# Kernel optimization log

Measured on AMD Instinct MI355X. Metric: run time of the kernel, lower is better.

Reference implementation:

```python
import jax, jax.numpy as jnp
import numpy as np


def _binop(ei, ej):
    # diagonal linear recurrence combine: (a_i, b_i) * (a_j, b_j) -> (a_j*a_i, a_j*b_i + b_j)
    ai, bi = ei
    aj, bj = ej
    return aj * ai, aj * bi + bj


def setup_inputs() -> dict:
    key = jax.random.key(0)
    ks = jax.random.split(key, 9)
    B_, T, D_in, D_out, N = 16, 2048, 512, 512, 512
    inp = {
        "input": jax.random.normal(ks[0], (B_, T, D_in), dtype=jnp.float32),
        "D": jax.random.normal(ks[1], (D_out, D_in), dtype=jnp.float32) / np.sqrt(D_in),
        "nu_log": jax.random.normal(ks[2], (N,), dtype=jnp.float32),
        "theta_log": jax.random.normal(ks[3], (N,), dtype=jnp.float32),
        "gamma_log": jax.random.normal(ks[4], (N,), dtype=jnp.float32),
        "B_re": jax.random.normal(ks[5], (N, D_in), dtype=jnp.float32) / np.sqrt(2 * D_in),
        "B_im": jax.random.normal(ks[6], (N, D_in), dtype=jnp.float32) / np.sqrt(2 * D_in),
        "C_re": jax.random.normal(ks[7], (D_out, N), dtype=jnp.float32) / np.sqrt(N),
        "C_im": jax.random.normal(ks[8], (D_out, N), dtype=jnp.float32) / np.sqrt(N),
    }
    return inp


def reference(input, D, nu_log, theta_log, gamma_log, B_re, B_im, C_re, C_im):
    # ss_params
    lam_abs = jnp.exp(-jnp.exp(nu_log))                      # [N]
    lam_phase = jnp.exp(theta_log)                           # [N]
    lam = lam_abs * (jnp.cos(lam_phase) + 1j * jnp.sin(lam_phase))  # complex [N]
    gamma = jnp.exp(gamma_log)                               # [N]
    Bc = (B_re + 1j * B_im) * gamma[:, None]                 # [N, D_in]
    Cc = C_re + 1j * C_im                                    # [D_out, N]

    # input projection: Bu_elements [batch, T, N] (complex)
    Bu = input.astype(Bc.dtype) @ Bc.T
    lam_el = jnp.broadcast_to(lam, Bu.shape)

    # parallel associative scan over time axis (initial state is zero)
    _, states = jax.lax.associative_scan(_binop, (lam_el, Bu), axis=1)

    # readout
    y = jnp.real(states @ Cc.T) + input @ D.T                # [batch, T, D_out]
    return y
```

## Files before the change

kernel.cpp:

```cpp
#include <hip/hip_runtime.h>
#include <hip/hip_fp16.h>

typedef _Float16 f16;
typedef __attribute__((ext_vector_type(8))) _Float16 f16x8;
typedef __attribute__((ext_vector_type(2))) _Float16 f16x2;
typedef __attribute__((ext_vector_type(16))) float f32x16;

#define B_SZ 16
#define T_SZ 2048
#define DIN 512
#define DOUT 512
#define N_SZ 512
#define M_SZ (B_SZ * T_SZ)
#define NCHUNK 16
#define LCHUNK 128

__device__ __forceinline__ void gload_lds16(const void* g, void* l) {
  __builtin_amdgcn_global_load_lds(
      (const __attribute__((address_space(1))) void*)g,
      (__attribute__((address_space(3))) void*)l, 16, 0, 0);
}


__global__ void prep_all(const float* __restrict__ nu_log,
                         const float* __restrict__ theta_log,
                         const float* __restrict__ gamma_log,
                         const float* __restrict__ B_re, const float* __restrict__ B_im,
                         const float* __restrict__ C_re, const float* __restrict__ C_im,
                         const float* __restrict__ Dm, const float* __restrict__ input,
                         float2* __restrict__ lam2, float2* __restrict__ lamL2,
                         f16* __restrict__ W1, f16* __restrict__ W2,
                         f16* __restrict__ A2) {
  int b = blockIdx.x;
  if (b < 2) {
    int n = b * 256 + threadIdx.x;
    float nu = expf(nu_log[n]);
    float ph = expf(theta_log[n]);
    float la = expf(-nu);
    lam2[n] = make_float2(la * cosf(ph), la * sinf(ph));
    float laL = expf(-nu * (float)LCHUNK);
    float phL = ph * (float)LCHUNK;
    lamL2[n] = make_float2(laL * cosf(phL), laL * sinf(phL));
  } else if (b < 2 + 2048) {
    int tid = (b - 2) * 256 + threadIdx.x;
    int np = tid >> 9;
    int d = tid & 511;
    int n = np >> 1;
    float g = expf(gamma_log[n]);
    const float* src = (np & 1) ? B_im : B_re;
    W1[(size_t)np * 512 + d] = (f16)(src[(size_t)n * 512 + d] * g);
  } else if (b < 2 + 2048 + 3072) {
    int tid = (b - 2050) * 256 + threadIdx.x;
    int j = tid / 1536;
    int k = tid - j * 1536;
    float v;
    if (k < 512)       v =  C_re[(size_t)j * 512 + k];
    else if (k < 1024) v = -C_im[(size_t)j * 512 + (k - 512)];
    else               v =  Dm[(size_t)j * 512 + (k - 1024)];
    W2[(size_t)j * 1536 + k] = (f16)v;
  } else {
    int tid = (b - 5122) * 256 + threadIdx.x;
    int m = tid >> 6;
    int d0 = (tid & 63) << 3;
    const float4* p = (const float4*)(input + (size_t)m * DIN + d0);
    float4 a = p[0], c = p[1];
    f16x8 h;
    h[0] = (f16)a.x; h[1] = (f16)a.y; h[2] = (f16)a.z; h[3] = (f16)a.w;
    h[4] = (f16)c.x; h[5] = (f16)c.y; h[6] = (f16)c.z; h[7] = (f16)c.w;
    *(f16x8*)(A2 + (size_t)m * 1536 + 1024 + d0) = h;
  }
}


__global__ void scan_a(const f16* __restrict__ Bu, const float2* __restrict__ lam2,
                       float2* __restrict__ S) {
  int tid = blockIdx.x * 256 + threadIdx.x;
  int n = tid & 511;
  int c = (tid >> 9) & (NCHUNK - 1);
  int b = tid >> 13;
  float2 l = lam2[n];
  const unsigned* bu = (const unsigned*)Bu + (size_t)(b * T_SZ + c * LCHUNK) * 512 + n;
  float sre = 0.f, sim = 0.f;
#pragma unroll 8
  for (int t = 0; t < LCHUNK; ++t) {
    unsigned u = bu[(size_t)t * 512];
    f16x2 h = __builtin_bit_cast(f16x2, u);
    float nre = l.x * sre - l.y * sim + (float)h.x;
    sim = l.x * sim + l.y * sre + (float)h.y;
    sre = nre;
  }
  S[(size_t)(b * NCHUNK + c) * 512 + n] = make_float2(sre, sim);
}

__global__ void scan_b(const float2* __restrict__ S, const float2* __restrict__ lamL2,
                       float2* __restrict__ Carry) {
  int tid = blockIdx.x * 256 + threadIdx.x;
  int n = tid & 511;
  int b = tid >> 9;
  float2 lL = lamL2[n];
  float cre = 0.f, cim = 0.f;
  for (int c = 0; c < NCHUNK; ++c) {
    size_t idx = (size_t)(b * NCHUNK + c) * 512 + n;
    Carry[idx] = make_float2(cre, cim);
    float2 s = S[idx];
    float nre = lL.x * cre - lL.y * cim + s.x;
    cim = lL.x * cim + lL.y * cre + s.y;
    cre = nre;
  }
}

__global__ void scan_c(const f16* __restrict__ Bu, const float2* __restrict__ lam2,
                       const float2* __restrict__ Carry, f16* __restrict__ A2) {
  int tid = blockIdx.x * 256 + threadIdx.x;
  int n = tid & 511;
  int c = (tid >> 9) & (NCHUNK - 1);
  int b = tid >> 13;
  float2 l = lam2[n];
  float2 car = Carry[(size_t)(b * NCHUNK + c) * 512 + n];
  float sre = car.x, sim = car.y;
  int m0 = b * T_SZ + c * LCHUNK;
  const unsigned* bu = (const unsigned*)Bu + (size_t)m0 * 512 + n;
  f16* outre = A2 + (size_t)m0 * 1536 + n;
#pragma unroll 4
  for (int t = 0; t < LCHUNK; ++t) {
    unsigned u = bu[(size_t)t * 512];
    f16x2 h = __builtin_bit_cast(f16x2, u);
    float nre = l.x * sre - l.y * sim + (float)h.x;
    sim = l.x * sim + l.y * sre + (float)h.y;
    sre = nre;
    outre[(size_t)t * 1536] = (f16)sre;
    outre[(size_t)t * 1536 + 512] = (f16)sim;
  }
}


template <typename CT>
__global__ __launch_bounds__(512, 2) void gemm256(
    const f16* __restrict__ A, int lda,
    const f16* __restrict__ Bm, int ldb,
    CT* __restrict__ C, int ldc, int K, int nxt) {
  extern __shared__ f16 smem[];
  const int tid = threadIdx.x;
  const int lane = tid & 63;
  const int wid = tid >> 6;
  const int wr = wid >> 2;
  const int wc = wid & 3;
  const int r32 = lane & 31;
  const int khalf = lane >> 5;
  const int key = r32 & 7;

  const int nwg = gridDim.x;
  const int id = blockIdx.x;
  const int swz = (id & 7) * (nwg >> 3) + (id >> 3);
  const int m0 = (swz / nxt) * 256;
  const int n0 = (swz % nxt) * 256;

  const int srow = tid >> 3;
  const int scol = ((tid & 7) ^ (srow & 7)) * 8;
  const int NT = K >> 6;

  f32x16 acc[4][2];
#pragma unroll
  for (int i = 0; i < 4; ++i)
#pragma unroll
    for (int j = 0; j < 2; ++j)
#pragma unroll
      for (int r = 0; r < 16; ++r) acc[i][j][r] = 0.f;

  auto stage = [&](int t) {
    f16* base = smem + (t & 1) * 32768;
    f16* dst = base + tid * 8;
    const f16* gA = A + (size_t)(m0 + srow) * lda + t * 64 + scol;
    const f16* gB = Bm + (size_t)(n0 + srow) * ldb + t * 64 + scol;
#pragma unroll
    for (int i = 0; i < 4; ++i) {
      gload_lds16(gA + (size_t)(i * 64) * lda, dst + i * 4096);
      gload_lds16(gB + (size_t)(i * 64) * ldb, dst + 16384 + i * 4096);
    }
  };

  stage(0);
  asm volatile("s_waitcnt vmcnt(0)" ::: "memory");
  __builtin_amdgcn_sched_barrier(0);
  __builtin_amdgcn_s_barrier();
  __builtin_amdgcn_sched_barrier(0);

  for (int t = 0; t < NT; ++t) {
    if (t + 1 < NT) stage(t + 1);
    const f16* bA = smem + (t & 1) * 32768;
    const f16* bB = bA + 16384;
#pragma unroll
    for (int ks = 0; ks < 4; ++ks) {
      const int so = ((ks * 2 + khalf) ^ key) * 8;
      f16x8 af[4], bf[2];
#pragma unroll
      for (int mi = 0; mi < 4; ++mi)
        af[mi] = *(const f16x8*)(bA + (wr * 128 + mi * 32 + r32) * 64 + so);
#pragma unroll
      for (int ni = 0; ni < 2; ++ni)
        bf[ni] = *(const f16x8*)(bB + (wc * 64 + ni * 32 + r32) * 64 + so);
#pragma unroll
      for (int mi = 0; mi < 4; ++mi)
#pragma unroll
        for (int ni = 0; ni < 2; ++ni)
          acc[mi][ni] = __builtin_amdgcn_mfma_f32_32x32x16_f16(
              af[mi], bf[ni], acc[mi][ni], 0, 0, 0);
    }
    asm volatile("s_waitcnt vmcnt(0)" ::: "memory");
    __builtin_amdgcn_sched_barrier(0);
    __builtin_amdgcn_s_barrier();
    __builtin_amdgcn_sched_barrier(0);
  }

#pragma unroll
  for (int mi = 0; mi < 4; ++mi)
#pragma unroll
    for (int ni = 0; ni < 2; ++ni)
#pragma unroll
      for (int r = 0; r < 16; ++r) {
        int row = m0 + wr * 128 + mi * 32 + (r & 3) + ((r >> 2) * 8) + khalf * 4;
        int col = n0 + wc * 64 + ni * 32 + r32;
        C[(size_t)row * ldc + col] = (CT)acc[mi][ni][r];
      }
}


extern "C" void kernel_launch(void* const* d_in, const int* in_sizes, int n_in,
                              void* d_out, int out_size, void* d_ws, size_t ws_size,
                              hipStream_t stream) {
  const float* input = (const float*)d_in[0];
  const float* Dmat = (const float*)d_in[1];
  const float* nu_log = (const float*)d_in[2];
  const float* theta_log = (const float*)d_in[3];
  const float* gamma_log = (const float*)d_in[4];
  const float* B_re = (const float*)d_in[5];
  const float* B_im = (const float*)d_in[6];
  const float* C_re = (const float*)d_in[7];
  const float* C_im = (const float*)d_in[8];
  float* y = (float*)d_out;

  char* ws = (char*)d_ws;
  size_t off = 0;
  auto alloc = [&](size_t bytes) {
    void* p = ws + off;
    off = (off + bytes + 255) & ~(size_t)255;
    return p;
  };
  float2* lam2 = (float2*)alloc(N_SZ * sizeof(float2));
  float2* lamL2 = (float2*)alloc(N_SZ * sizeof(float2));
  f16* W1 = (f16*)alloc((size_t)2 * N_SZ * DIN * 2);
  f16* W2 = (f16*)alloc((size_t)DOUT * 1536 * 2);
  f16* A2 = (f16*)alloc((size_t)M_SZ * 1536 * 2);
  f16* Bu = (f16*)alloc((size_t)M_SZ * 2 * N_SZ * 2);
  float2* S = (float2*)alloc((size_t)B_SZ * NCHUNK * N_SZ * sizeof(float2));
  float2* Carry = (float2*)alloc((size_t)B_SZ * NCHUNK * N_SZ * sizeof(float2));

  const int shmem = 131072;
  {
    auto* g16 = gemm256<f16>;
    auto* g32 = gemm256<float>;
    hipFuncSetAttribute((const void*)g16,
                        hipFuncAttributeMaxDynamicSharedMemorySize, shmem);
    hipFuncSetAttribute((const void*)g32,
                        hipFuncAttributeMaxDynamicSharedMemorySize, shmem);
  }

  prep_all<<<13314, 256, 0, stream>>>(nu_log, theta_log, gamma_log, B_re, B_im,
                                      C_re, C_im, Dmat, input, lam2, lamL2, W1, W2, A2);

  gemm256<f16><<<512, 512, shmem, stream>>>(A2 + 1024, 1536, W1, 512, Bu, 1024, 512, 4);

  scan_a<<<(B_SZ * NCHUNK * N_SZ) / 256, 256, 0, stream>>>(Bu, lam2, S);
  scan_b<<<(B_SZ * N_SZ) / 256, 256, 0, stream>>>(S, lamL2, Carry);
  scan_c<<<(B_SZ * NCHUNK * N_SZ) / 256, 256, 0, stream>>>(Bu, lam2, Carry, A2);

  gemm256<float><<<256, 512, shmem, stream>>>(A2, 1536, W2, 1536, y, 512, 1536, 2);
}
```

Baseline: 164.5 us.

## Replace double-buffered GEMM with 4-slot K=32 ring buffer, prefetch depth two

Restructures the GEMM main loop to use four LDS slots of K=32 tiles instead of two K=64 slots. Loads are issued two stages ahead and a partial vmcnt wait is used, so global-to-LDS copies overlap more with MFMA work. It also adds a new XOR swizzle for the 32-wide rows and raises wave priority around the MFMA block. The trade-off is one barrier per 32-K step, which doubles the barrier count, and less MFMA work per barrier.

```diff
diff --git a/kernel.cpp b/kernel.cpp
--- a/kernel.cpp
+++ b/kernel.cpp
@@ -135,7 +135,7 @@
 
 
 template <typename CT>
-__global__ __launch_bounds__(512, 2) void gemm256(
+__global__ __launch_bounds__(512, 2) void gemm_ring(
     const f16* __restrict__ A, int lda,
     const f16* __restrict__ Bm, int ldb,
     CT* __restrict__ C, int ldc, int K, int nxt) {
@@ -147,7 +147,7 @@
   const int wc = wid & 3;
   const int r32 = lane & 31;
   const int khalf = lane >> 5;
-  const int key = r32 & 7;
+  const int key = (r32 & 3) ^ ((r32 >> 2) & 3);
 
   const int nwg = gridDim.x;
   const int id = blockIdx.x;
@@ -155,9 +155,9 @@
   const int m0 = (swz / nxt) * 256;
   const int n0 = (swz % nxt) * 256;
 
-  const int srow = tid >> 3;
-  const int scol = ((tid & 7) ^ (srow & 7)) * 8;
-  const int NT = K >> 6;
+  const int srow = tid >> 2;
+  const int scol = ((tid & 3) ^ (srow & 3) ^ ((srow >> 2) & 3)) * 8;
+  const int NG = K >> 5;
 
   f32x16 acc[4][2];
 #pragma unroll
@@ -167,49 +167,55 @@
 #pragma unroll
       for (int r = 0; r < 16; ++r) acc[i][j][r] = 0.f;
 
-  auto stage = [&](int t) {
-    f16* base = smem + (t & 1) * 32768;
-    f16* dst = base + tid * 8;
-    const f16* gA = A + (size_t)(m0 + srow) * lda + t * 64 + scol;
-    const f16* gB = Bm + (size_t)(n0 + srow) * ldb + t * 64 + scol;
-#pragma unroll
-    for (int i = 0; i < 4; ++i) {
-      gload_lds16(gA + (size_t)(i * 64) * lda, dst + i * 4096);
-      gload_lds16(gB + (size_t)(i * 64) * ldb, dst + 16384 + i * 4096);
-    }
+  auto stage = [&](int g) {
+    f16* dst = smem + (g & 3) * 16384 + tid * 8;
+    const f16* gA = A + (size_t)(m0 + srow) * lda + g * 32 + scol;
+    const f16* gB = Bm + (size_t)(n0 + srow) * ldb + g * 32 + scol;
+    gload_lds16(gA, dst);
+    gload_lds16(gA + (size_t)128 * lda, dst + 4096);
+    gload_lds16(gB, dst + 8192);
+    gload_lds16(gB + (size_t)128 * ldb, dst + 12288);
   };
 
   stage(0);
-  asm volatile("s_waitcnt vmcnt(0)" ::: "memory");
-  __builtin_amdgcn_sched_barrier(0);
-  __builtin_amdgcn_s_barrier();
-  __builtin_amdgcn_sched_barrier(0);
-
-  for (int t = 0; t < NT; ++t) {
-    if (t + 1 < NT) stage(t + 1);
-    const f16* bA = smem + (t & 1) * 32768;
-    const f16* bB = bA + 16384;
-#pragma unroll
-    for (int ks = 0; ks < 4; ++ks) {
-      const int so = ((ks * 2 + khalf) ^ key) * 8;
-      f16x8 af[4], bf[2];
-#pragma unroll
-      for (int mi = 0; mi < 4; ++mi)
-        af[mi] = *(const f16x8*)(bA + (wr * 128 + mi * 32 + r32) * 64 + so);
-#pragma unroll
-      for (int ni = 0; ni < 2; ++ni)
-        bf[ni] = *(const f16x8*)(bB + (wc * 64 + ni * 32 + r32) * 64 + so);
-#pragma unroll
-      for (int mi = 0; mi < 4; ++mi)
-#pragma unroll
-        for (int ni = 0; ni < 2; ++ni)
-          acc[mi][ni] = __builtin_amdgcn_mfma_f32_32x32x16_f16(
-              af[mi], bf[ni], acc[mi][ni], 0, 0, 0);
-    }
-    asm volatile("s_waitcnt vmcnt(0)" ::: "memory");
+  stage(1);
+
+  for (int g = 0; g < NG; ++g) {
+    if (g + 1 < NG)
+      asm volatile("s_waitcnt vmcnt(4)" ::: "memory");
+    else
+      asm volatile("s_waitcnt vmcnt(0)" ::: "memory");
     __builtin_amdgcn_sched_barrier(0);
     __builtin_amdgcn_s_barrier();
     __builtin_amdgcn_sched_barrier(0);
+    if (g + 2 < NG) stage(g + 2);
+
+    const f16* sa = smem + (g & 3) * 16384 + (wr * 128) * 32;
+    const f16* sb = smem + (g & 3) * 16384 + 8192 + (wc * 64) * 32;
+    f16x8 af[4][2], bf[2][2];
+#pragma unroll
+    for (int mi = 0; mi < 4; ++mi)
+#pragma unroll
+      for (int k = 0; k < 2; ++k)
+        af[mi][k] = *(const f16x8*)(sa + (mi * 32 + r32) * 32 +
+                                    (((k * 2 + khalf) ^ key) * 8));
+#pragma unroll
+    for (int ni = 0; ni < 2; ++ni)
+#pragma unroll
+      for (int k = 0; k < 2; ++k)
+        bf[ni][k] = *(const f16x8*)(sb + (ni * 32 + r32) * 32 +
+                                    (((k * 2 + khalf) ^ key) * 8));
+
+    __builtin_amdgcn_s_setprio(1);
+#pragma unroll
+    for (int k = 0; k < 2; ++k)
+#pragma unroll
+      for (int mi = 0; mi < 4; ++mi)
+#pragma unroll
+        for (int ni = 0; ni < 2; ++ni)
+          acc[mi][ni] = __builtin_amdgcn_mfma_f32_32x32x16_f16(
+              af[mi][k], bf[ni][k], acc[mi][ni], 0, 0, 0);
+    __builtin_amdgcn_s_setprio(0);
   }
 
 #pragma unroll
@@ -257,8 +263,8 @@
 
   const int shmem = 131072;
   {
-    auto* g16 = gemm256<f16>;
-    auto* g32 = gemm256<float>;
+    auto* g16 = gemm_ring<f16>;
+    auto* g32 = gemm_ring<float>;
     hipFuncSetAttribute((const void*)g16,
                         hipFuncAttributeMaxDynamicSharedMemorySize, shmem);
     hipFuncSetAttribute((const void*)g32,
@@ -268,11 +274,11 @@
   prep_all<<<13314, 256, 0, stream>>>(nu_log, theta_log, gamma_log, B_re, B_im,
                                       C_re, C_im, Dmat, input, lam2, lamL2, W1, W2, A2);
 
-  gemm256<f16><<<512, 512, shmem, stream>>>(A2 + 1024, 1536, W1, 512, Bu, 1024, 512, 4);
+  gemm_ring<f16><<<512, 512, shmem, stream>>>(A2 + 1024, 1536, W1, 512, Bu, 1024, 512, 4);
 
   scan_a<<<(B_SZ * NCHUNK * N_SZ) / 256, 256, 0, stream>>>(Bu, lam2, S);
   scan_b<<<(B_SZ * N_SZ) / 256, 256, 0, stream>>>(S, lamL2, Carry);
   scan_c<<<(B_SZ * NCHUNK * N_SZ) / 256, 256, 0, stream>>>(Bu, lam2, Carry, A2);
 
-  gemm256<float><<<256, 512, shmem, stream>>>(A2, 1536, W2, 1536, y, 512, 1536, 2);
-}
+  gemm_ring<float><<<256, 512, shmem, stream>>>(A2, 1536, W2, 1536, y, 512, 1536, 2);
+}
```

New measurement: 167.8 us. About the same (+2.0%).
